# Optimization experiments

Hardware: AMD Instinct MI355X
Metric: run time of the kernel (lower is better)

## Reference

```python
import jax, jax.numpy as jnp
import numpy as np

NUM_HEADS = 8

def setup_inputs() -> dict:
    key = jax.random.key(0)
    k1, k2, k3, k4 = jax.random.split(key, 4)
    B, N, C = 2, 4096, 768
    x = jax.random.normal(k1, (B, N, C), dtype=jnp.float32)
    w_qkv = jax.random.normal(k2, (C, 3 * C), dtype=jnp.float32) * (C ** -0.5)
    w_proj = jax.random.normal(k3, (C, C), dtype=jnp.float32) * (C ** -0.5)
    b_proj = jax.random.normal(k4, (C,), dtype=jnp.float32) * 0.02
    return {"x": x, "w_qkv": w_qkv, "w_proj": w_proj, "b_proj": b_proj}

def reference(x, w_qkv, w_proj, b_proj):
    B, N, C = x.shape
    H = NUM_HEADS
    Dh = C // H
    scale = Dh ** -0.5
    # qkv: [B, N, 3C] -> [B, N, 3, H, Dh] -> [3, B, H, N, Dh]
    qkv = (x @ w_qkv).reshape(B, N, 3, H, Dh).transpose(2, 0, 3, 1, 4)
    q, k, v = qkv[0], qkv[1], qkv[2]
    attn = jnp.einsum('bhqd,bhkd->bhqk', q, k) * scale  # [B,H,N,N]
    attn = jax.nn.softmax(attn, axis=-1)
    out = jnp.einsum('bhqk,bhkd->bhqd', attn, v)        # [B,H,N,Dh]
    out = out.transpose(0, 2, 1, 3).reshape(B, N, C)
    return out @ w_proj + b_proj
```

## Files before the change

### kernel.cpp

```cpp
#include <hip/hip_runtime.h>
#include <hip/hip_bf16.h>

typedef __attribute__((ext_vector_type(8))) short short8;
typedef __attribute__((ext_vector_type(4))) short short4v;
typedef __attribute__((ext_vector_type(4))) float f32x4;
typedef __attribute__((ext_vector_type(16))) float f32x16;

#define MFMA16(a,b,c) __builtin_amdgcn_mfma_f32_16x16x32_bf16(a,b,c,0,0,0)
#define MFMA32(a,b,c) __builtin_amdgcn_mfma_f32_32x32x16_bf16(a,b,c,0,0,0)

__device__ __forceinline__ unsigned short f2b_rne(float f){
  union { float f; unsigned int u; } v; v.f = f;
  unsigned int u = v.u;
  return (unsigned short)((u + 0x7FFFu + ((u >> 16) & 1u)) >> 16);
}

__device__ __forceinline__ f32x16 zero16(){
  f32x16 z;
  #pragma unroll
  for (int i = 0; i < 16; ++i) z[i] = 0.f;
  return z;
}

__global__ __launch_bounds__(256) void k_cvt(const float* __restrict__ in,
                                             unsigned short* __restrict__ out, int n8){
  int i = blockIdx.x * 256 + threadIdx.x;
  if (i >= n8) return;
  const float4* p = (const float4*)in + (size_t)i * 2;
  float4 a = p[0], b = p[1];
  short8 o;
  o[0] = (short)f2b_rne(a.x); o[1] = (short)f2b_rne(a.y);
  o[2] = (short)f2b_rne(a.z); o[3] = (short)f2b_rne(a.w);
  o[4] = (short)f2b_rne(b.x); o[5] = (short)f2b_rne(b.y);
  o[6] = (short)f2b_rne(b.z); o[7] = (short)f2b_rne(b.w);
  *((short8*)out + i) = o;
}

__global__ void k_transpose_cvt(const float* __restrict__ in, unsigned short* __restrict__ out,
                                int R, int Cc){
  __shared__ unsigned short tile[32][33];
  int c0 = blockIdx.x * 32, r0 = blockIdx.y * 32;
  int tx = threadIdx.x, ty = threadIdx.y;
  #pragma unroll
  for (int i = 0; i < 32; i += 8)
    tile[ty + i][tx] = f2b_rne(in[(size_t)(r0 + ty + i) * Cc + c0 + tx]);
  __syncthreads();
  #pragma unroll
  for (int i = 0; i < 32; i += 8)
    out[(size_t)(c0 + ty + i) * R + r0 + tx] = tile[tx][ty + i];
}

__global__ __launch_bounds__(256) void k_gemm_qkv(
    const unsigned short* __restrict__ A,
    const unsigned short* __restrict__ Bt,
    unsigned short* __restrict__ qbuf,
    unsigned short* __restrict__ kbuf,
    unsigned short* __restrict__ vtb)
{
  __shared__ short As[128 * 40];
  __shared__ short Bs[128 * 40];
  int m0 = blockIdx.x * 128, n0 = blockIdx.y * 128;
  int t = threadIdx.x, l = t & 63, w = t >> 6;
  int lr = l & 15, lh = l >> 4;
  int wr = w >> 1, wc = w & 1;

  int row0 = t >> 2, cs0 = t & 3;
  int row1 = row0 + 64;
  const unsigned short* ga0 = A  + (size_t)(m0 + row0) * 768 + cs0 * 8;
  const unsigned short* ga1 = A  + (size_t)(m0 + row1) * 768 + cs0 * 8;
  const unsigned short* gb0 = Bt + (size_t)(n0 + row0) * 768 + cs0 * 8;
  const unsigned short* gb1 = Bt + (size_t)(n0 + row1) * 768 + cs0 * 8;
  short* la0 = As + row0 * 40 + cs0 * 8;
  short* la1 = As + row1 * 40 + cs0 * 8;
  short* lb0 = Bs + row0 * 40 + cs0 * 8;
  short* lb1 = Bs + row1 * 40 + cs0 * 8;

  f32x4 acc[4][4];
  f32x4 z4 = {0.f, 0.f, 0.f, 0.f};
  #pragma unroll
  for (int mf = 0; mf < 4; ++mf)
    #pragma unroll
    for (int nf = 0; nf < 4; ++nf) acc[mf][nf] = z4;

  short8 ra0 = *(const short8*)ga0;
  short8 ra1 = *(const short8*)ga1;
  short8 rb0 = *(const short8*)gb0;
  short8 rb1 = *(const short8*)gb1;

  for (int kt = 0; kt < 24; ++kt){
    __syncthreads();
    *(short8*)la0 = ra0; *(short8*)la1 = ra1;
    *(short8*)lb0 = rb0; *(short8*)lb1 = rb1;
    __syncthreads();
    if (kt < 23){
      ra0 = *(const short8*)(ga0 + (kt + 1) * 32);
      ra1 = *(const short8*)(ga1 + (kt + 1) * 32);
      rb0 = *(const short8*)(gb0 + (kt + 1) * 32);
      rb1 = *(const short8*)(gb1 + (kt + 1) * 32);
    }
    short8 af[4], bfm[4];
    #pragma unroll
    for (int mf = 0; mf < 4; ++mf)
      af[mf] = *(const short8*)(As + (wr * 64 + mf * 16 + lr) * 40 + lh * 8);
    #pragma unroll
    for (int nf = 0; nf < 4; ++nf)
      bfm[nf] = *(const short8*)(Bs + (wc * 64 + nf * 16 + lr) * 40 + lh * 8);
    #pragma unroll
    for (int mf = 0; mf < 4; ++mf)
      #pragma unroll
      for (int nf = 0; nf < 4; ++nf)
        acc[mf][nf] = MFMA16(af[mf], bfm[nf], acc[mf][nf]);
  }

  const float qscale = 0.10206207261596577f * 1.4426950408889634f;
  int three = n0 / 768;
  int b_ = m0 >> 12;
  int ntok0 = m0 & 4095;
  #pragma unroll
  for (int nf = 0; nf < 4; ++nf){
    int gcol = n0 + wc * 64 + nf * 16 + lr;
    int jj = gcol - three * 768;
    int h = jj / 96;
    int dh = jj - h * 96;
    #pragma unroll
    for (int mf = 0; mf < 4; ++mf){
      int ntok = ntok0 + wr * 64 + mf * 16 + lh * 4;
      if (three == 0){
        unsigned short* dst = qbuf + (size_t)(b_ * 8 + h) * 4096 * 96;
        #pragma unroll
        for (int r = 0; r < 4; ++r)
          dst[(size_t)(ntok + r) * 96 + dh] = f2b_rne(acc[mf][nf][r] * qscale);
      } else if (three == 1){
        unsigned short* dst = kbuf + (size_t)(b_ * 8 + h) * 4096 * 96;
        #pragma unroll
        for (int r = 0; r < 4; ++r)
          dst[(size_t)(ntok + r) * 96 + dh] = f2b_rne(acc[mf][nf][r]);
      } else {
        short4v sv;
        #pragma unroll
        for (int r = 0; r < 4; ++r) sv[r] = (short)f2b_rne(acc[mf][nf][r]);
        *(short4v*)(vtb + ((size_t)(b_ * 8 + h) * 96 + dh) * 4096 + ntok) = sv;
      }
    }
  }
}

__global__ __launch_bounds__(512) __attribute__((amdgpu_waves_per_eu(2, 2)))
void k_attn5(
    const unsigned short* __restrict__ qb,
    const unsigned short* __restrict__ kb,
    const unsigned short* __restrict__ vtb,
    unsigned short* __restrict__ ao)
{
  __shared__ short lds[27136];
  const int bh = blockIdx.x;
  const int qt = blockIdx.y;
  const int tid = threadIdx.x;
  const int ln = tid & 63, wid = tid >> 6;
  const int qc = ln & 31, hi = ln >> 5;
  const int set = wid >> 2, qquad = wid & 3;
  const int q0 = qt * 256 + qquad * 64;

  const unsigned short* qbase = qb  + (size_t)bh * 4096 * 96;
  const unsigned short* kbase = kb  + (size_t)bh * 4096 * 96;
  const unsigned short* vbase = vtb + (size_t)bh * 96 * 4096;

  short8 qf[2][6];
  #pragma unroll
  for (int g = 0; g < 2; ++g)
    #pragma unroll
    for (int kw = 0; kw < 6; ++kw)
      qf[g][kw] = *(const short8*)(qbase + (size_t)(q0 + g * 32 + qc) * 96 + kw * 16 + hi * 8);

  const unsigned short* gp[6]; int loff[6];
  #pragma unroll
  for (int j = 0; j < 3; ++j){
    int ck = tid + j * 512;
    int s = (ck >= 768) ? 1 : 0;
    int cc = ck - s * 768;
    int r = cc / 12, cl = cc - r * 12;
    gp[j] = kbase + (size_t)(s * 64 + r) * 96 + cl * 8;
    loff[j] = s * 6656 + r * 104 + cl * 8;
  }
  #pragma unroll
  for (int j = 3; j < 6; ++j){
    int cv = tid + (j - 3) * 512;
    int s = (cv >= 768) ? 1 : 0;
    int cc = cv - s * 768;
    int r = cc >> 3, cl = cc & 7;
    gp[j] = vbase + (size_t)r * 4096 + s * 64 + cl * 8;
    loff[j] = 13312 + s * 6912 + r * 72 + cl * 8;
  }

  short8 rs[6];
  #pragma unroll
  for (int j = 0; j < 6; ++j) rs[j] = *(const short8*)gp[j];
  #pragma unroll
  for (int j = 0; j < 3; ++j) gp[j] += 12288;
  #pragma unroll
  for (int j = 3; j < 6; ++j) gp[j] += 128;
  #pragma unroll
  for (int j = 0; j < 6; ++j) *(short8*)(lds + loff[j]) = rs[j];

  f32x16 oacc[2][3];
  #pragma unroll
  for (int g = 0; g < 2; ++g)
    #pragma unroll
    for (int dt = 0; dt < 3; ++dt) oacc[g][dt] = zero16();
  float mr[2] = {-1e30f, -1e30f}, lr_[2] = {0.f, 0.f};

  const short* Kb = lds + set * 6656 + qc * 104 + hi * 8;
  const short* Vb = lds + 13312 + set * 6912 + qc * 72 + hi * 8;

#define CVTPK(d, lo_, hi_) asm("v_cvt_pk_bf16_f32 %0, %1, %2" : "=v"(d) : "v"(lo_), "v"(hi_))
#define PLSWAP(x_, y_)     asm("v_permlane32_swap_b32 %0, %1" : "+v"(x_), "+v"(y_))

#define PA_H(pa_, s_)                                                                    \
  {                                                                                      \
    unsigned int a_, b_;                                                                 \
    union { unsigned int u[4]; short8 s; } pk_;                                          \
    CVTPK(a_, s_[0],  s_[1]);  CVTPK(b_, s_[4],  s_[5]);  PLSWAP(a_, b_); pk_.u[0]=a_; pk_.u[2]=b_; \
    CVTPK(a_, s_[2],  s_[3]);  CVTPK(b_, s_[6],  s_[7]);  PLSWAP(a_, b_); pk_.u[1]=a_; pk_.u[3]=b_; \
    pa_[0] = pk_.s;                                                                      \
    CVTPK(a_, s_[8],  s_[9]);  CVTPK(b_, s_[12], s_[13]); PLSWAP(a_, b_); pk_.u[0]=a_; pk_.u[2]=b_; \
    CVTPK(a_, s_[10], s_[11]); CVTPK(b_, s_[14], s_[15]); PLSWAP(a_, b_); pk_.u[1]=a_; pk_.u[3]=b_; \
    pa_[1] = pk_.s;                                                                      \
  }

#define SOFTMAX_H(g_, s_)                                                                \
  {                                                                                      \
    float t0 = fmaxf(s_[0], s_[1]),  t1 = fmaxf(s_[2], s_[3]);                           \
    float t2 = fmaxf(s_[4], s_[5]),  t3 = fmaxf(s_[6], s_[7]);                           \
    t0 = fmaxf(t0, fmaxf(s_[8],  s_[9]));  t1 = fmaxf(t1, fmaxf(s_[10], s_[11]));        \
    t2 = fmaxf(t2, fmaxf(s_[12], s_[13])); t3 = fmaxf(t3, fmaxf(s_[14], s_[15]));        \
    float tmax = fmaxf(fmaxf(t0, t1), fmaxf(t2, t3));                                    \
    tmax = fmaxf(tmax, __shfl_xor(tmax, 32, 64));                                        \
    if (!__all(tmax - mr[g_] <= 8.0f)){                                                  \
      float mn = fmaxf(mr[g_], tmax);                                                    \
      float al = exp2f(mr[g_] - mn);                                                     \
      _Pragma("unroll")                                                                  \
      for (int dt = 0; dt < 3; ++dt)                                                     \
        _Pragma("unroll")                                                                 \
        for (int r = 0; r < 16; ++r) oacc[g_][dt][r] *= al;                              \
      lr_[g_] *= al; mr[g_] = mn;                                                        \
    }                                                                                    \
    float p0 = 0.f, p1 = 0.f, p2 = 0.f, p3 = 0.f;                                        \
    _Pragma("unroll")                                                                    \
    for (int r = 0; r < 16; r += 4){                                                     \
      s_[r]   = exp2f(s_[r]   - mr[g_]); p0 += s_[r];                                    \
      s_[r+1] = exp2f(s_[r+1] - mr[g_]); p1 += s_[r+1];                                  \
      s_[r+2] = exp2f(s_[r+2] - mr[g_]); p2 += s_[r+2];                                  \
      s_[r+3] = exp2f(s_[r+3] - mr[g_]); p3 += s_[r+3];                                  \
    }                                                                                    \
    float psum = (p0 + p1) + (p2 + p3);                                                  \
    psum += __shfl_xor(psum, 32, 64);                                                    \
    lr_[g_] += psum;                                                                     \
  }

  for (int ss = 0; ss < 32; ++ss){
    __syncthreads();

    {
      f32x16 s0 = zero16(), s1 = zero16();
      __builtin_amdgcn_s_setprio(1);
      #pragma unroll
      for (int kw = 0; kw < 6; ++kw){
        short8 kf = *(const short8*)(Kb + kw * 16);
        s0 = MFMA32(kf, qf[0][kw], s0);
        s1 = MFMA32(kf, qf[1][kw], s1);
      }
      __builtin_amdgcn_s_setprio(0);

      SOFTMAX_H(0, s0)
      short8 pa0[2];
      PA_H(pa0, s0)
      SOFTMAX_H(1, s1)
      short8 pa1[2];
      PA_H(pa1, s1)

      if (ss < 31){
        #pragma unroll
        for (int j = 0; j < 3; ++j){ rs[j] = *(const short8*)gp[j]; gp[j] += 12288; }
      }

      __builtin_amdgcn_s_setprio(1);
      #pragma unroll
      for (int dt = 0; dt < 3; ++dt){
        #pragma unroll
        for (int w = 0; w < 2; ++w){
          short8 vf = *(const short8*)(Vb + dt * 2304 + w * 16);
          oacc[0][dt] = MFMA32(vf, pa0[w], oacc[0][dt]);
          oacc[1][dt] = MFMA32(vf, pa1[w], oacc[1][dt]);
        }
      }
      __builtin_amdgcn_s_setprio(0);
    }

    {
      f32x16 s0 = zero16(), s1 = zero16();
      __builtin_amdgcn_s_setprio(1);
      #pragma unroll
      for (int kw = 0; kw < 6; ++kw){
        short8 kf = *(const short8*)(Kb + 3328 + kw * 16);
        s0 = MFMA32(kf, qf[0][kw], s0);
        s1 = MFMA32(kf, qf[1][kw], s1);
      }
      __builtin_amdgcn_s_setprio(0);

      SOFTMAX_H(0, s0)
      short8 pa0[2];
      PA_H(pa0, s0)
      SOFTMAX_H(1, s1)
      short8 pa1[2];
      PA_H(pa1, s1)

      if (ss < 31){
        #pragma unroll
        for (int j = 3; j < 6; ++j){ rs[j] = *(const short8*)gp[j]; gp[j] += 128; }
      }

      __builtin_amdgcn_s_setprio(1);
      #pragma unroll
      for (int dt = 0; dt < 3; ++dt){
        #pragma unroll
        for (int w = 0; w < 2; ++w){
          short8 vf = *(const short8*)(Vb + dt * 2304 + 32 + w * 16);
          oacc[0][dt] = MFMA32(vf, pa0[w], oacc[0][dt]);
          oacc[1][dt] = MFMA32(vf, pa1[w], oacc[1][dt]);
        }
      }
      __builtin_amdgcn_s_setprio(0);
    }

    __syncthreads();
    if (ss < 31){
      #pragma unroll
      for (int j = 0; j < 6; ++j) *(short8*)(lds + loff[j]) = rs[j];
    }
  }

  float* fl = (float*)lds;
  #pragma unroll
  for (int g = 0; g < 2; ++g){
    __syncthreads();
    if (set == 1){
      #pragma unroll
      for (int dt = 0; dt < 3; ++dt)
        #pragma unroll
        for (int r = 0; r < 16; ++r)
          fl[qquad * 3072 + dt * 1024 + r * 64 + ln] = oacc[g][dt][r];
      fl[12288 + qquad * 64 + ln] = mr[g];
      fl[12544 + qquad * 64 + ln] = lr_[g];
    }
    __syncthreads();
    if (set == 0){
      float m1v = fl[12288 + qquad * 64 + ln];
      float l1v = fl[12544 + qquad * 64 + ln];
      float M  = fmaxf(mr[g], m1v);
      float w0 = exp2f(mr[g] - M), w1 = exp2f(m1v - M);
      lr_[g] = w0 * lr_[g] + w1 * l1v;
      #pragma unroll
      for (int dt = 0; dt < 3; ++dt)
        #pragma unroll
        for (int r = 0; r < 16; ++r)
          oacc[g][dt][r] = w0 * oacc[g][dt][r] + w1 * fl[qquad * 3072 + dt * 1024 + r * 64 + ln];
    }
  }

  if (set == 0){
    int b_ = bh >> 3, h = bh & 7;
    #pragma unroll
    for (int g = 0; g < 2; ++g){
      float inv = 1.0f / lr_[g];
      unsigned short* orow = ao + (size_t)(b_ * 4096 + q0 + g * 32 + qc) * 768 + h * 96;
      #pragma unroll
      for (int dt = 0; dt < 3; ++dt)
        #pragma unroll
        for (int g4 = 0; g4 < 4; ++g4){
          short4v sv;
          #pragma unroll
          for (int r = 0; r < 4; ++r) sv[r] = (short)f2b_rne(oacc[g][dt][g4 * 4 + r] * inv);
          *(short4v*)(orow + dt * 32 + g4 * 8 + hi * 4) = sv;
        }
    }
  }
#undef CVTPK
#undef PLSWAP
#undef PA_H
#undef SOFTMAX_H
}

__global__ __launch_bounds__(256) void k_gemm_proj(
    const unsigned short* __restrict__ A,
    const unsigned short* __restrict__ Bt,
    const float* __restrict__ bias,
    float* __restrict__ out)
{
  __shared__ short As[128 * 40];
  __shared__ short Bs[128 * 40];
  int m0 = blockIdx.x * 128, n0 = blockIdx.y * 128;
  int t = threadIdx.x, l = t & 63, w = t >> 6;
  int lr = l & 15, lh = l >> 4;
  int wr = w >> 1, wc = w & 1;

  int row0 = t >> 2, cs0 = t & 3;
  int row1 = row0 + 64;
  const unsigned short* ga0 = A  + (size_t)(m0 + row0) * 768 + cs0 * 8;
  const unsigned short* ga1 = A  + (size_t)(m0 + row1) * 768 + cs0 * 8;
  const unsigned short* gb0 = Bt + (size_t)(n0 + row0) * 768 + cs0 * 8;
  const unsigned short* gb1 = Bt + (size_t)(n0 + row1) * 768 + cs0 * 8;
  short* la0 = As + row0 * 40 + cs0 * 8;
  short* la1 = As + row1 * 40 + cs0 * 8;
  short* lb0 = Bs + row0 * 40 + cs0 * 8;
  short* lb1 = Bs + row1 * 40 + cs0 * 8;

  f32x4 acc[4][4];
  f32x4 z4 = {0.f, 0.f, 0.f, 0.f};
  #pragma unroll
  for (int mf = 0; mf < 4; ++mf)
    #pragma unroll
    for (int nf = 0; nf < 4; ++nf) acc[mf][nf] = z4;

  short8 ra0 = *(const short8*)ga0;
  short8 ra1 = *(const short8*)ga1;
  short8 rb0 = *(const short8*)gb0;
  short8 rb1 = *(const short8*)gb1;

  for (int kt = 0; kt < 24; ++kt){
    __syncthreads();
    *(short8*)la0 = ra0; *(short8*)la1 = ra1;
    *(short8*)lb0 = rb0; *(short8*)lb1 = rb1;
    __syncthreads();
    if (kt < 23){
      ra0 = *(const short8*)(ga0 + (kt + 1) * 32);
      ra1 = *(const short8*)(ga1 + (kt + 1) * 32);
      rb0 = *(const short8*)(gb0 + (kt + 1) * 32);
      rb1 = *(const short8*)(gb1 + (kt + 1) * 32);
    }
    short8 af[4], bfm[4];
    #pragma unroll
    for (int mf = 0; mf < 4; ++mf)
      af[mf] = *(const short8*)(As + (wr * 64 + mf * 16 + lr) * 40 + lh * 8);
    #pragma unroll
    for (int nf = 0; nf < 4; ++nf)
      bfm[nf] = *(const short8*)(Bs + (wc * 64 + nf * 16 + lr) * 40 + lh * 8);
    #pragma unroll
    for (int mf = 0; mf < 4; ++mf)
      #pragma unroll
      for (int nf = 0; nf < 4; ++nf)
        acc[mf][nf] = MFMA16(af[mf], bfm[nf], acc[mf][nf]);
  }

  #pragma unroll
  for (int nf = 0; nf < 4; ++nf){
    int gcol = n0 + wc * 64 + nf * 16 + lr;
    float bb = bias[gcol];
    #pragma unroll
    for (int mf = 0; mf < 4; ++mf){
      int grow = m0 + wr * 64 + mf * 16 + lh * 4;
      #pragma unroll
      for (int r = 0; r < 4; ++r)
        out[(size_t)(grow + r) * 768 + gcol] = acc[mf][nf][r] + bb;
    }
  }
}

extern "C" void kernel_launch(void* const* d_in, const int* in_sizes, int n_in,
                              void* d_out, int out_size, void* d_ws, size_t ws_size,
                              hipStream_t stream) {
  const float* x      = (const float*)d_in[0];
  const float* w_qkv  = (const float*)d_in[1];
  const float* w_proj = (const float*)d_in[2];
  const float* b_proj = (const float*)d_in[3];
  float* out = (float*)d_out;
  char* ws = (char*)d_ws;

  unsigned short* xb     = (unsigned short*)(ws);
  unsigned short* wqkvt  = (unsigned short*)(ws + 12582912);
  unsigned short* wprojt = (unsigned short*)(ws + 16121856);
  unsigned short* qbuf   = (unsigned short*)(ws + 17301504);
  unsigned short* kbuf   = (unsigned short*)(ws + 29884416);
  unsigned short* vtb    = (unsigned short*)(ws + 42467328);
  unsigned short* aob    = xb;

  k_cvt<<<3072, 256, 0, stream>>>(x, xb, 786432);
  k_transpose_cvt<<<dim3(72, 24), dim3(32, 8), 0, stream>>>(w_qkv, wqkvt, 768, 2304);
  k_transpose_cvt<<<dim3(24, 24), dim3(32, 8), 0, stream>>>(w_proj, wprojt, 768, 768);
  k_gemm_qkv<<<dim3(64, 18), 256, 0, stream>>>(xb, wqkvt, qbuf, kbuf, vtb);
  k_attn5<<<dim3(16, 16), 512, 0, stream>>>(qbuf, kbuf, vtb, aob);
  k_gemm_proj<<<dim3(64, 6), 256, 0, stream>>>(aob, wprojt, b_proj, out);
}
```

Measured before the change: 228.4 us.

## Halve per-wave query rows in attention to raise occupancy and grid size

Each wave in the attention kernel now handles 32 query rows instead of 64, so the block covers 128 queries and the grid doubles to 512 blocks. Register use for Q fragments, output accumulators and softmax state is halved, and the waves-per-EU hint goes from 2 to 4 to allow more resident waves. In exchange, every K/V tile loaded into LDS feeds half as many MFMAs, so K/V traffic per unit of work doubles, and there are fewer independent MFMA chains per wave to hide latency.

```diff
diff --git a/kernel.cpp b/kernel.cpp
--- a/kernel.cpp
+++ b/kernel.cpp
@@ -145,8 +145,8 @@
   }
 }
 
-__global__ __launch_bounds__(512) __attribute__((amdgpu_waves_per_eu(2, 2)))
-void k_attn5(
+__global__ __launch_bounds__(512) __attribute__((amdgpu_waves_per_eu(4)))
+void k_attn6(
     const unsigned short* __restrict__ qb,
     const unsigned short* __restrict__ kb,
     const unsigned short* __restrict__ vtb,
@@ -159,18 +159,16 @@
   const int ln = tid & 63, wid = tid >> 6;
   const int qc = ln & 31, hi = ln >> 5;
   const int set = wid >> 2, qquad = wid & 3;
-  const int q0 = qt * 256 + qquad * 64;
+  const int q0 = qt * 128 + qquad * 32;
 
   const unsigned short* qbase = qb  + (size_t)bh * 4096 * 96;
   const unsigned short* kbase = kb  + (size_t)bh * 4096 * 96;
   const unsigned short* vbase = vtb + (size_t)bh * 96 * 4096;
 
-  short8 qf[2][6];
-  #pragma unroll
-  for (int g = 0; g < 2; ++g)
-    #pragma unroll
-    for (int kw = 0; kw < 6; ++kw)
-      qf[g][kw] = *(const short8*)(qbase + (size_t)(q0 + g * 32 + qc) * 96 + kw * 16 + hi * 8);
+  short8 qf[6];
+  #pragma unroll
+  for (int kw = 0; kw < 6; ++kw)
+    qf[kw] = *(const short8*)(qbase + (size_t)(q0 + qc) * 96 + kw * 16 + hi * 8);
 
   const unsigned short* gp[6]; int loff[6];
   #pragma unroll
@@ -202,12 +200,10 @@
   #pragma unroll
   for (int j = 0; j < 6; ++j) *(short8*)(lds + loff[j]) = rs[j];
 
-  f32x16 oacc[2][3];
-  #pragma unroll
-  for (int g = 0; g < 2; ++g)
-    #pragma unroll
-    for (int dt = 0; dt < 3; ++dt) oacc[g][dt] = zero16();
-  float mr[2] = {-1e30f, -1e30f}, lr_[2] = {0.f, 0.f};
+  f32x16 oacc[3];
+  #pragma unroll
+  for (int dt = 0; dt < 3; ++dt) oacc[dt] = zero16();
+  float mr = -1e30f, lr_ = 0.f;
 
   const short* Kb = lds + set * 6656 + qc * 104 + hi * 8;
   const short* Vb = lds + 13312 + set * 6912 + qc * 72 + hi * 8;
@@ -227,7 +223,7 @@
     pa_[1] = pk_.s;                                                                      \
   }
 
-#define SOFTMAX_H(g_, s_)                                                                \
+#define SOFTMAX_H(s_)                                                                    \
   {                                                                                      \
     float t0 = fmaxf(s_[0], s_[1]),  t1 = fmaxf(s_[2], s_[3]);                           \
     float t2 = fmaxf(s_[4], s_[5]),  t3 = fmaxf(s_[6], s_[7]);                           \
@@ -235,48 +231,44 @@
     t2 = fmaxf(t2, fmaxf(s_[12], s_[13])); t3 = fmaxf(t3, fmaxf(s_[14], s_[15]));        \
     float tmax = fmaxf(fmaxf(t0, t1), fmaxf(t2, t3));                                    \
     tmax = fmaxf(tmax, __shfl_xor(tmax, 32, 64));                                        \
-    if (!__all(tmax - mr[g_] <= 8.0f)){                                                  \
-      float mn = fmaxf(mr[g_], tmax);                                                    \
-      float al = exp2f(mr[g_] - mn);                                                     \
+    if (!__all(tmax - mr <= 8.0f)){                                                      \
+      float mn = fmaxf(mr, tmax);                                                        \
+      float al = exp2f(mr - mn);                                                         \
       _Pragma("unroll")                                                                  \
       for (int dt = 0; dt < 3; ++dt)                                                     \
         _Pragma("unroll")                                                                 \
-        for (int r = 0; r < 16; ++r) oacc[g_][dt][r] *= al;                              \
-      lr_[g_] *= al; mr[g_] = mn;                                                        \
+        for (int r = 0; r < 16; ++r) oacc[dt][r] *= al;                                  \
+      lr_ *= al; mr = mn;                                                                \
     }                                                                                    \
     float p0 = 0.f, p1 = 0.f, p2 = 0.f, p3 = 0.f;                                        \
     _Pragma("unroll")                                                                    \
     for (int r = 0; r < 16; r += 4){                                                     \
-      s_[r]   = exp2f(s_[r]   - mr[g_]); p0 += s_[r];                                    \
-      s_[r+1] = exp2f(s_[r+1] - mr[g_]); p1 += s_[r+1];                                  \
-      s_[r+2] = exp2f(s_[r+2] - mr[g_]); p2 += s_[r+2];                                  \
-      s_[r+3] = exp2f(s_[r+3] - mr[g_]); p3 += s_[r+3];                                  \
+      s_[r]   = exp2f(s_[r]   - mr); p0 += s_[r];                                        \
+      s_[r+1] = exp2f(s_[r+1] - mr); p1 += s_[r+1];                                      \
+      s_[r+2] = exp2f(s_[r+2] - mr); p2 += s_[r+2];                                      \
+      s_[r+3] = exp2f(s_[r+3] - mr); p3 += s_[r+3];                                      \
     }                                                                                    \
     float psum = (p0 + p1) + (p2 + p3);                                                  \
     psum += __shfl_xor(psum, 32, 64);                                                    \
-    lr_[g_] += psum;                                                                     \
+    lr_ += psum;                                                                         \
   }
 
   for (int ss = 0; ss < 32; ++ss){
     __syncthreads();
 
     {
-      f32x16 s0 = zero16(), s1 = zero16();
+      f32x16 s0 = zero16();
       __builtin_amdgcn_s_setprio(1);
       #pragma unroll
       for (int kw = 0; kw < 6; ++kw){
         short8 kf = *(const short8*)(Kb + kw * 16);
-        s0 = MFMA32(kf, qf[0][kw], s0);
-        s1 = MFMA32(kf, qf[1][kw], s1);
+        s0 = MFMA32(kf, qf[kw], s0);
       }
       __builtin_amdgcn_s_setprio(0);
 
-      SOFTMAX_H(0, s0)
+      SOFTMAX_H(s0)
       short8 pa0[2];
       PA_H(pa0, s0)
-      SOFTMAX_H(1, s1)
-      short8 pa1[2];
-      PA_H(pa1, s1)
 
       if (ss < 31){
         #pragma unroll
@@ -289,30 +281,25 @@
         #pragma unroll
         for (int w = 0; w < 2; ++w){
           short8 vf = *(const short8*)(Vb + dt * 2304 + w * 16);
-          oacc[0][dt] = MFMA32(vf, pa0[w], oacc[0][dt]);
-          oacc[1][dt] = MFMA32(vf, pa1[w], oacc[1][dt]);
+          oacc[dt] = MFMA32(vf, pa0[w], oacc[dt]);
         }
       }
       __builtin_amdgcn_s_setprio(0);
     }
 
     {
-      f32x16 s0 = zero16(), s1 = zero16();
+      f32x16 s0 = zero16();
       __builtin_amdgcn_s_setprio(1);
       #pragma unroll
       for (int kw = 0; kw < 6; ++kw){
         short8 kf = *(const short8*)(Kb + 3328 + kw * 16);
-        s0 = MFMA32(kf, qf[0][kw], s0);
-        s1 = MFMA32(kf, qf[1][kw], s1);
+        s0 = MFMA32(kf, qf[kw], s0);
       }
       __builtin_amdgcn_s_setprio(0);
 
-      SOFTMAX_H(0, s0)
+      SOFTMAX_H(s0)
       short8 pa0[2];
       PA_H(pa0, s0)
-      SOFTMAX_H(1, s1)
-      short8 pa1[2];
-      PA_H(pa1, s1)
 
       if (ss < 31){
         #pragma unroll
@@ -325,8 +312,7 @@
         #pragma unroll
         for (int w = 0; w < 2; ++w){
           short8 vf = *(const short8*)(Vb + dt * 2304 + 32 + w * 16);
-          oacc[0][dt] = MFMA32(vf, pa0[w], oacc[0][dt]);
-          oacc[1][dt] = MFMA32(vf, pa1[w], oacc[1][dt]);
+          oacc[dt] = MFMA32(vf, pa0[w], oacc[dt]);
         }
       }
       __builtin_amdgcn_s_setprio(0);
@@ -340,49 +326,45 @@
   }
 
   float* fl = (float*)lds;
-  #pragma unroll
-  for (int g = 0; g < 2; ++g){
+  {
     __syncthreads();
     if (set == 1){
       #pragma unroll
       for (int dt = 0; dt < 3; ++dt)
         #pragma unroll
         for (int r = 0; r < 16; ++r)
-          fl[qquad * 3072 + dt * 1024 + r * 64 + ln] = oacc[g][dt][r];
-      fl[12288 + qquad * 64 + ln] = mr[g];
-      fl[12544 + qquad * 64 + ln] = lr_[g];
+          fl[qquad * 3072 + dt * 1024 + r * 64 + ln] = oacc[dt][r];
+      fl[12288 + qquad * 64 + ln] = mr;
+      fl[12544 + qquad * 64 + ln] = lr_;
     }
     __syncthreads();
     if (set == 0){
       float m1v = fl[12288 + qquad * 64 + ln];
       float l1v = fl[12544 + qquad * 64 + ln];
-      float M  = fmaxf(mr[g], m1v);
-      float w0 = exp2f(mr[g] - M), w1 = exp2f(m1v - M);
-      lr_[g] = w0 * lr_[g] + w1 * l1v;
+      float M  = fmaxf(mr, m1v);
+      float w0 = exp2f(mr - M), w1 = exp2f(m1v - M);
+      lr_ = w0 * lr_ + w1 * l1v;
       #pragma unroll
       for (int dt = 0; dt < 3; ++dt)
         #pragma unroll
         for (int r = 0; r < 16; ++r)
-          oacc[g][dt][r] = w0 * oacc[g][dt][r] + w1 * fl[qquad * 3072 + dt * 1024 + r * 64 + ln];
+          oacc[dt][r] = w0 * oacc[dt][r] + w1 * fl[qquad * 3072 + dt * 1024 + r * 64 + ln];
     }
   }
 
   if (set == 0){
     int b_ = bh >> 3, h = bh & 7;
-    #pragma unroll
-    for (int g = 0; g < 2; ++g){
-      float inv = 1.0f / lr_[g];
-      unsigned short* orow = ao + (size_t)(b_ * 4096 + q0 + g * 32 + qc) * 768 + h * 96;
-      #pragma unroll
-      for (int dt = 0; dt < 3; ++dt)
-        #pragma unroll
-        for (int g4 = 0; g4 < 4; ++g4){
-          short4v sv;
-          #pragma unroll
-          for (int r = 0; r < 4; ++r) sv[r] = (short)f2b_rne(oacc[g][dt][g4 * 4 + r] * inv);
-          *(short4v*)(orow + dt * 32 + g4 * 8 + hi * 4) = sv;
-        }
-    }
+    float inv = 1.0f / lr_;
+    unsigned short* orow = ao + (size_t)(b_ * 4096 + q0 + qc) * 768 + h * 96;
+    #pragma unroll
+    for (int dt = 0; dt < 3; ++dt)
+      #pragma unroll
+      for (int g4 = 0; g4 < 4; ++g4){
+        short4v sv;
+        #pragma unroll
+        for (int r = 0; r < 4; ++r) sv[r] = (short)f2b_rne(oacc[dt][g4 * 4 + r] * inv);
+        *(short4v*)(orow + dt * 32 + g4 * 8 + hi * 4) = sv;
+      }
   }
 #undef CVTPK
 #undef PLSWAP
@@ -487,6 +469,6 @@
   k_transpose_cvt<<<dim3(72, 24), dim3(32, 8), 0, stream>>>(w_qkv, wqkvt, 768, 2304);
   k_transpose_cvt<<<dim3(24, 24), dim3(32, 8), 0, stream>>>(w_proj, wprojt, 768, 768);
   k_gemm_qkv<<<dim3(64, 18), 256, 0, stream>>>(xb, wqkvt, qbuf, kbuf, vtb);
-  k_attn5<<<dim3(16, 16), 512, 0, stream>>>(qbuf, kbuf, vtb, aob);
+  k_attn6<<<dim3(16, 32), 512, 0, stream>>>(qbuf, kbuf, vtb, aob);
   k_gemm_proj<<<dim3(64, 6), 256, 0, stream>>>(aob, wprojt, b_proj, out);
 }
```

New measurement: 238.3 us. 1.04x slower.
